# Optimization experiments

Measured on AMD Instinct MI355X. Metric: run time of the kernel, lower is better.

Reference implementation:

```python
import jax, jax.numpy as jnp
import numpy as np

N = 50000      # n_samples (nodes)
F = 128        # n_features
H = 32         # hidden_dim
C = 16         # code_dim
DEG = 32       # avg degree
E = N * DEG + N  # random edges + self loops


def setup_inputs() -> dict:
    key = jax.random.key(0)
    ks = jax.random.split(key, 9)
    src = jax.random.randint(ks[0], (N * DEG,), 0, N, dtype=jnp.int32)
    dst = jax.random.randint(ks[1], (N * DEG,), 0, N, dtype=jnp.int32)
    loops = jnp.arange(N, dtype=jnp.int32)
    edge_src = jnp.concatenate([src, loops])
    edge_dst = jnp.concatenate([dst, loops])
    # symmetric normalization D^{-1/2} (A+I) D^{-1/2} on the edge list
    deg = jax.ops.segment_sum(jnp.ones((E,), jnp.float32), edge_dst, num_segments=N)
    deg = jnp.maximum(deg, 1.0)
    edge_w = jax.lax.rsqrt(deg[edge_src] * deg[edge_dst])
    rand_u = jax.random.uniform(ks[2], (N, C), jnp.float32)  # torch.rand_like
    def w(k, i, o):
        return jax.random.normal(k, (i, o), jnp.float32) * (1.0 / np.sqrt(i))
    return {
        'x': jax.random.normal(ks[3], (N, F), jnp.float32),
        'edge_src': edge_src, 'edge_dst': edge_dst, 'edge_w': edge_w,
        'rand_u': rand_u,
        'W1': w(ks[4], F, H), 'Wm': w(ks[5], H, C), 'Ws': w(ks[6], H, C),
        'Wd': w(ks[7], C, H), 'Wo': w(ks[8], H, F),
    }


def _gcn(x, W, edge_src, edge_dst, edge_w):
    # KipfAndWillingConv: spmm(A_norm, x @ W)
    support = x @ W                               # [N, out]
    msgs = edge_w[:, None] * support[edge_src]    # [E, out]
    return jax.ops.segment_sum(msgs, edge_dst, num_segments=N)


def reference(x, edge_src, edge_dst, edge_w, rand_u, W1, Wm, Ws, Wd, Wo):
    gcn = lambda h, W: _gcn(h, W, edge_src, edge_dst, edge_w)
    hidden = jax.nn.relu(gcn(x, W1))
    means = gcn(hidden, Wm)
    std = jax.nn.elu(gcn(hidden, Ws)) + 1.0
    encoded = means + std * rand_u                # uniform reparameterization
    decoded = jax.nn.relu(gcn(encoded, Wd))
    prediction = jax.nn.relu(gcn(decoded, Wo))
    return (prediction, means, std)
```

## Files before the change

### kernel.cpp

```cpp
#include <hip/hip_runtime.h>
#include <hip/hip_bf16.h>
#include <hip/hip_fp16.h>

typedef unsigned int u32;
typedef unsigned short u16;
typedef unsigned long long u64;

#define NBIN 512
#define BSH 7
#define BCAP 36
#define CHUNK 4096
#define PAD 80
#define NG  (PAD/8)
#define HB 128

__global__ __launch_bounds__(64) void k_init(int* __restrict__ ovf_cnt,
                                             u32* __restrict__ h0, u32* __restrict__ h1,
                                             u32* __restrict__ henc, int N) {
  const int t = threadIdx.x;
  if (t == 0) *ovf_cnt = 0;
  if (t < 16) h0[(size_t)N * 16 + t] = 0;
  if (t < 16) h1[(size_t)N * 16 + t] = 0;
  if (t < 8)  henc[(size_t)N * 8 + t] = 0;
}

__global__ __launch_bounds__(512) void k_bin(const int* __restrict__ src, const int* __restrict__ dst,
                                             int E2, u32* __restrict__ binned, int* __restrict__ blkcnt,
                                             u32* __restrict__ ovf, int* __restrict__ ovf_cnt, int ovfcap) {
  __shared__ int curs[NBIN];
  const int p = blockIdx.x;
  const int base = p * CHUNK;
  const int len = min(CHUNK, E2 - base);
  const int t = threadIdx.x;
  const int lane = t & 63;
  for (int i = t; i < NBIN; i += 512) curs[i] = 0;
  __syncthreads();
  const u32 blkBase = (u32)p * (NBIN * BCAP);
  for (int i = t; i < len; i += 512) {
    int d = dst[base + i];
    u32 e = ((u32)d << 16) | (u32)src[base + i];
    int b = d >> BSH;
    int pos = atomicAdd(&curs[b], 1);
    if (pos < BCAP) binned[blkBase + (u32)b * BCAP + pos] = e;
    u64 om = __ballot(pos >= BCAP);
    if (om) {
      int leader = __ffsll((long long)om) - 1;
      int ob = 0;
      if (lane == leader) ob = atomicAdd(ovf_cnt, (int)__popcll(om));
      ob = __shfl(ob, leader);
      if (pos >= BCAP) {
        int oi = ob + (int)__popcll(om & ((1ull << lane) - 1ull));
        if (oi < ovfcap) ovf[oi] = e;
      }
    }
  }
  __syncthreads();
  for (int b = t; b < NBIN; b += 512) blkcnt[p * NBIN + b] = min(curs[b], BCAP);
}

__global__ __launch_bounds__(512) void k_sort(const u32* __restrict__ binned, const int* __restrict__ blkcnt,
                                              int nblk, const u32* __restrict__ ovf,
                                              const int* __restrict__ ovf_cnt, int N,
                                              u16* __restrict__ csr, int* __restrict__ cur) {
  __shared__ __attribute__((aligned(16))) u16 scsr[HB * PAD];
  __shared__ int cnt[HB];
  const int bin = blockIdx.x;
  const int lo = bin << BSH;
  if (lo >= N) return;
  const int hi = min(lo + HB, N);
  const int H = hi - lo;
  const int t = threadIdx.x;
  const int w = t >> 6, lane = t & 63;
  const u32 sent2 = ((u32)N << 16) | (u32)N;
  for (int i = t; i < HB * PAD / 2; i += 512) ((u32*)scsr)[i] = sent2;
  for (int i = t; i < HB; i += 512) cnt[i] = 0;
  __syncthreads();
  const int per = (nblk + 7) / 8;
  const int c0 = w * per;
  const int c1 = min(nblk, c0 + per);
  const int s = lane >> 3;
  const int k = lane & 7;
  for (int p = c0; p < c1; p += 8) {
    const int myp = p + s;
    int len = 0; u32 sb = 0;
    if (myp < c1) {
      len = blkcnt[myp * NBIN + bin];
      sb = ((u32)myp * NBIN + (u32)bin) * BCAP;
    }
    for (int i = k; i < len; i += 8) {
      u32 e = binned[sb + i];
      int d = (int)(e >> 16);
      int pos = atomicAdd(&cnt[d - lo], 1);
      if (pos < PAD) scsr[(d - lo) * PAD + pos] = (u16)(e & 0xffffu);
    }
  }
  const int onum = min(*ovf_cnt, 1 << 19);
  for (int i = t; i < onum; i += 512) {
    u32 e = ovf[i];
    int d = (int)(e >> 16);
    if (d >= lo && d < hi) {
      int pos = atomicAdd(&cnt[d - lo], 1);
      if (pos < PAD) scsr[(d - lo) * PAD + pos] = (u16)(e & 0xffffu);
    }
  }
  __syncthreads();
  if (H == HB) {
    const uint4* s4 = (const uint4*)scsr;
    uint4* d4 = (uint4*)(csr + (size_t)lo * PAD);
    for (int i = t; i < HB * PAD / 8; i += 512) d4[i] = s4[i];
  } else {
    for (int i = t; i < H * (PAD / 8); i += 512) {
      int node = i / (PAD / 8), q = i % (PAD / 8);
      ((uint4*)(csr + (size_t)(lo + node) * PAD))[q] = ((const uint4*)(scsr + node * PAD))[q];
    }
  }
  for (int i = t; i < H; i += 512) cur[lo + i] = cnt[i];
}

__device__ __forceinline__ void acc8(uint4 v, float* a) {
  const __half2* h = reinterpret_cast<const __half2*>(&v);
#pragma unroll
  for (int p = 0; p < 4; ++p) {
    float2 f = __half22float2(h[p]);
    a[2 * p] += f.x;
    a[2 * p + 1] += f.y;
  }
}
__device__ __forceinline__ uint4 pack8h(const float* v) {
  uint4 r;
  __half2* h = reinterpret_cast<__half2*>(&r);
#pragma unroll
  for (int p = 0; p < 4; ++p) h[p] = __floats2half2_rn(v[2 * p], v[2 * p + 1]);
  return r;
}
__device__ __forceinline__ uint2 pack4h(const float* v) {
  uint2 r;
  __half2* h = reinterpret_cast<__half2*>(&r);
  h[0] = __floats2half2_rn(v[0], v[1]);
  h[1] = __floats2half2_rn(v[2], v[3]);
  return r;
}
__device__ __forceinline__ u32 pack2h(float a, float b) {
  __half2 h = __floats2half2_rn(a, b);
  return *reinterpret_cast<u32*>(&h);
}

template <int LPN, int XD>
__device__ __forceinline__ void gather_split(const u16* __restrict__ csr, const int* __restrict__ cur,
                                             const float* __restrict__ dinv, const uint4* __restrict__ supv,
                                             int g, int cg, int half, float* acc, float& dg_out) {
  const int len = min(cur[g], PAD);
  const u16* c = csr + (size_t)g * PAD;
  ushort4 idx[NG];
#pragma unroll
  for (int j = 0; j < NG; ++j) idx[j] = *(const ushort4*)(c + 8 * j + 4 * half);
#pragma unroll
  for (int p = 0; p < 8; ++p) acc[p] = 0.f;
  if (half == 0) acc8(supv[(size_t)g * LPN + cg], acc);
#pragma unroll
  for (int j = 0; j < NG; ++j) {
    if (8 * j + 4 * half < len) {
      acc8(supv[(size_t)idx[j].x * LPN + cg], acc);
      acc8(supv[(size_t)idx[j].y * LPN + cg], acc);
      acc8(supv[(size_t)idx[j].z * LPN + cg], acc);
      acc8(supv[(size_t)idx[j].w * LPN + cg], acc);
    }
  }
  float dg = dinv[g];
#pragma unroll
  for (int p = 0; p < 8; ++p) acc[p] += __shfl_xor(acc[p], XD);
  dg_out = dg;
#pragma unroll
  for (int p = 0; p < 8; ++p) acc[p] *= dg;
}

__global__ __launch_bounds__(256) void k_spmm_relu(const u16* __restrict__ csr, const int* __restrict__ cur,
                                                   const float* __restrict__ dinv,
                                                   const uint4* __restrict__ sup, uint4* __restrict__ out, int N) {
  int g = blockIdx.x * 32 + (int)(threadIdx.x >> 3);
  int sub = threadIdx.x & 7;
  int half = sub >> 2, cg = sub & 3;
  if (g >= N) return;
  float a[8], dg;
  gather_split<4, 4>(csr, cur, dinv, sup, g, cg, half, a, dg);
  if (half == 0) {
#pragma unroll
    for (int p = 0; p < 8; ++p) a[p] = dg * fmaxf(a[p], 0.f);
    out[(size_t)g * 4 + cg] = pack8h(a);
  }
}

__global__ __launch_bounds__(256) void k_spmm_ms(const u16* __restrict__ csr, const int* __restrict__ cur,
                                                  const float* __restrict__ dinv,
                                                  const uint4* __restrict__ sup,
                                                  const float* __restrict__ Wm, const float* __restrict__ Ws,
                                                  const float* __restrict__ ru,
                                                  u32* __restrict__ enc,
                                                  float* __restrict__ o_means, float* __restrict__ o_std, int N) {
  __shared__ float w[32 * 32];
  __shared__ float aggT[32][33];
  const int t = threadIdx.x;
  for (int i = t; i < 32 * 32; i += 256) {
    int k = i >> 5, j = i & 31;
    w[i] = (j < 16) ? Wm[k * 16 + j] : Ws[k * 16 + (j - 16)];
  }
  const int n = t >> 3;
  const int sub = t & 7;
  const int half = sub >> 2, cg = sub & 3;
  const int g = blockIdx.x * 32 + n;
  const bool act = g < N;
  float dg = 0.f, a[8];
  if (act) {
    gather_split<4, 4>(csr, cur, dinv, sup, g, cg, half, a, dg);
    if (half == 0) {
#pragma unroll
      for (int p = 0; p < 8; ++p) aggT[n][cg * 8 + p] = a[p];
    }
  }
  __syncthreads();
  if (act) {
    const int q = sub;
    float2 rm = make_float2(0.f, 0.f), rs = make_float2(0.f, 0.f);
    for (int k = 0; k < 32; ++k) {
      float rv = aggT[n][k];
      const float2* wr = (const float2*)&w[k * 32];
      float2 wm = wr[q], wsv = wr[8 + q];
      rm.x += rv * wm.x; rm.y += rv * wm.y;
      rs.x += rv * wsv.x; rs.y += rv * wsv.y;
    }
    ((float2*)o_means)[(size_t)g * 8 + q] = rm;
    rs.x = ((rs.x > 0.f) ? rs.x : expm1f(rs.x)) + 1.0f;
    rs.y = ((rs.y > 0.f) ? rs.y : expm1f(rs.y)) + 1.0f;
    ((float2*)o_std)[(size_t)g * 8 + q] = rs;
    float2 uu = ((const float2*)ru)[(size_t)g * 8 + q];
    enc[(size_t)g * 8 + q] = pack2h(dg * (rm.x + rs.x * uu.x), dg * (rm.y + rs.y * uu.y));
  }
}

__global__ __launch_bounds__(256) void k_spmm_d(const u16* __restrict__ csr, const int* __restrict__ cur,
                                                 const float* __restrict__ dinv,
                                                 const uint4* __restrict__ sup,
                                                 const float* __restrict__ Wd,
                                                 uint2* __restrict__ out, int N) {
  __shared__ float w[16 * 32];
  __shared__ float aggT[64][17];
  const int t = threadIdx.x;
  for (int i = t; i < 16 * 32; i += 256) w[i] = Wd[i];
  const int n = t >> 2;
  const int sub = t & 3;
  const int half = sub >> 1, cg = sub & 1;
  const int g = blockIdx.x * 64 + n;
  const bool act = g < N;
  float dg = 0.f, a[8];
  if (act) {
    gather_split<2, 2>(csr, cur, dinv, sup, g, cg, half, a, dg);
    if (half == 0) {
#pragma unroll
      for (int p = 0; p < 8; ++p) aggT[n][cg * 8 + p] = a[p];
    }
  }
  __syncthreads();
  if (act) {
    const int q = sub;
    float4 r0 = make_float4(0.f, 0.f, 0.f, 0.f), r1 = r0;
    for (int k = 0; k < 16; ++k) {
      float rv = aggT[n][k];
      const float4* wr = (const float4*)&w[k * 32];
      float4 w0 = wr[q], w1 = wr[q + 4];
      r0.x += rv * w0.x; r0.y += rv * w0.y; r0.z += rv * w0.z; r0.w += rv * w0.w;
      r1.x += rv * w1.x; r1.y += rv * w1.y; r1.z += rv * w1.z; r1.w += rv * w1.w;
    }
    float v[4];
    v[0] = dg * fmaxf(r0.x, 0.f); v[1] = dg * fmaxf(r0.y, 0.f);
    v[2] = dg * fmaxf(r0.z, 0.f); v[3] = dg * fmaxf(r0.w, 0.f);
    out[(size_t)g * 8 + q] = pack4h(v);
    v[0] = dg * fmaxf(r1.x, 0.f); v[1] = dg * fmaxf(r1.y, 0.f);
    v[2] = dg * fmaxf(r1.z, 0.f); v[3] = dg * fmaxf(r1.w, 0.f);
    out[(size_t)g * 8 + q + 4] = pack4h(v);
  }
}

__global__ __launch_bounds__(256) void k_spmm_o(const u16* __restrict__ csr, const int* __restrict__ cur,
                                                 const float* __restrict__ dinv,
                                                 const uint4* __restrict__ sup,
                                                 const float* __restrict__ Wo,
                                                 float* __restrict__ out, int N) {
  __shared__ float w[32 * 128];
  __shared__ float aggT[32][33];
  const int t = threadIdx.x;
  for (int i = t; i < 32 * 128; i += 256) w[i] = Wo[i];
  const int n = t >> 3;
  const int sub = t & 7;
  const int half = sub >> 2, cg = sub & 3;
  const int g = blockIdx.x * 32 + n;
  const bool act = g < N;
  float dg, a[8];
  if (act) {
    gather_split<4, 4>(csr, cur, dinv, sup, g, cg, half, a, dg);
    if (half == 0) {
#pragma unroll
      for (int p = 0; p < 8; ++p) aggT[n][cg * 8 + p] = a[p];
    }
  }
  __syncthreads();
  if (act) {
    const int q = sub;
    float4 r4[4];
#pragma unroll
    for (int h = 0; h < 4; ++h) r4[h] = make_float4(0.f, 0.f, 0.f, 0.f);
    for (int k = 0; k < 32; ++k) {
      float rv = aggT[n][k];
      const float4* wr = (const float4*)&w[k * 128];
#pragma unroll
      for (int h = 0; h < 4; ++h) {
        float4 wv = wr[q + 8 * h];
        r4[h].x += rv * wv.x; r4[h].y += rv * wv.y;
        r4[h].z += rv * wv.z; r4[h].w += rv * wv.w;
      }
    }
    float4* orow = (float4*)(out + (size_t)g * 128);
#pragma unroll
    for (int h = 0; h < 4; ++h)
      orow[q + 8 * h] = make_float4(fmaxf(r4[h].x, 0.f), fmaxf(r4[h].y, 0.f),
                                    fmaxf(r4[h].z, 0.f), fmaxf(r4[h].w, 0.f));
  }
}

__global__ __launch_bounds__(256) void k_mm1(const float* __restrict__ x, const float* __restrict__ W1,
                                             const int* __restrict__ cur, float* __restrict__ dinv,
                                             uint4* __restrict__ out, int N) {
  __shared__ float w[128 * 32];
  for (int i = threadIdx.x; i < 128 * 32; i += 256) w[i] = W1[i];
  __syncthreads();
  int n = blockIdx.x * 256 + threadIdx.x;
  if (n >= N) return;
  float dn = rsqrtf((float)(cur[n] + 1));
  dinv[n] = dn;
  const float4* xr = (const float4*)(x + (size_t)n * 128);
  float acc[32];
#pragma unroll
  for (int j = 0; j < 32; ++j) acc[j] = 0.f;
  for (int kb = 0; kb < 32; ++kb) {
    float4 p = xr[kb];
    float xe[4] = {p.x, p.y, p.z, p.w};
#pragma unroll
    for (int h = 0; h < 4; ++h) {
      float xv = xe[h];
      const float4* wr = (const float4*)&w[(kb * 4 + h) * 32];
#pragma unroll
      for (int q = 0; q < 8; ++q) {
        float4 a = wr[q];
        acc[q * 4 + 0] += xv * a.x; acc[q * 4 + 1] += xv * a.y;
        acc[q * 4 + 2] += xv * a.z; acc[q * 4 + 3] += xv * a.w;
      }
    }
  }
#pragma unroll
  for (int j = 0; j < 32; ++j) acc[j] *= dn;
  uint4* o = out + (size_t)n * 4;
#pragma unroll
  for (int q = 0; q < 4; ++q) o[q] = pack8h(&acc[q * 8]);
}

extern "C" void kernel_launch(void* const* d_in, const int* in_sizes, int n_in,
                              void* d_out, int out_size, void* d_ws, size_t ws_size,
                              hipStream_t stream) {
  const float* x  = (const float*)d_in[0];
  const int* esrc = (const int*)d_in[1];
  const int* edst = (const int*)d_in[2];
  const float* ru = (const float*)d_in[4];
  const float* W1 = (const float*)d_in[5];
  const float* Wm = (const float*)d_in[6];
  const float* Ws = (const float*)d_in[7];
  const float* Wd = (const float*)d_in[8];
  const float* Wo = (const float*)d_in[9];
  const int N = in_sizes[0] / 128;
  const int E = in_sizes[1];
  const int E2 = E - N;

  const int nblk = (E2 + CHUNK - 1) / CHUNK;
  const int ovfcap = 1 << 19;

  char* ws = (char*)d_ws;
  size_t off = 0;
  auto alloc = [&](size_t bytes) {
    void* p = ws + off;
    off = (off + bytes + 255) & ~(size_t)255;
    return p;
  };
  u16*   csr     = (u16*)alloc((size_t)N * PAD * 2);
  u32*   binned  = (u32*)alloc((size_t)nblk * NBIN * BCAP * 4);
  int*   blkcnt  = (int*)alloc((size_t)nblk * NBIN * 4);
  u32*   ovf     = (u32*)alloc((size_t)ovfcap * 4);
  int*   ovf_cnt = (int*)alloc(256);
  int*   cur     = (int*)alloc((size_t)N * 4);
  float* dinv    = (float*)alloc((size_t)N * 4);
  uint4* h0      = (uint4*)alloc((size_t)(N + 1) * 32 * 2);
  uint4* h1      = (uint4*)alloc((size_t)(N + 1) * 32 * 2);
  u32*   henc    = (u32*)alloc((size_t)(N + 1) * 16 * 2);

  float* out_pred  = (float*)d_out;
  float* out_means = out_pred + (size_t)N * 128;
  float* out_std   = out_means + (size_t)N * 16;

  const int nb = (N + 255) / 256;
  const int sortBlocks = (N + HB - 1) / HB;
  const int g32 = (N + 31) / 32;
  const int g64 = (N + 63) / 64;

  k_init<<<1, 64, 0, stream>>>(ovf_cnt, (u32*)h0, (u32*)h1, henc, N);
  k_bin<<<nblk, 512, 0, stream>>>(esrc, edst, E2, binned, blkcnt, ovf, ovf_cnt, ovfcap);
  k_sort<<<sortBlocks, 512, 0, stream>>>(binned, blkcnt, nblk, ovf, ovf_cnt, N, csr, cur);

  k_mm1<<<nb, 256, 0, stream>>>(x, W1, cur, dinv, h0, N);
  k_spmm_relu<<<g32, 256, 0, stream>>>(csr, cur, dinv, h0, h1, N);
  k_spmm_ms<<<g32, 256, 0, stream>>>(csr, cur, dinv, h1, Wm, Ws, ru,
                                     henc, out_means, out_std, N);
  k_spmm_d<<<g64, 256, 0, stream>>>(csr, cur, dinv, (const uint4*)henc, Wd,
                                    (uint2*)h0, N);
  k_spmm_o<<<g32, 256, 0, stream>>>(csr, cur, dinv, h0, Wo, out_pred, N);
}
```

Baseline: 128.3 us.

## Fuse first matmul into CSR sort kernel and split gathers across four lanes

The x@W1 projection and the degree normalisation are folded into the tail of k_sort. Each block reuses its shared CSR buffer to hold W1 and computes its 128 nodes with four threads per node, combined by lane shuffles. This removes a separate kernel launch and a reread of the degree counts. The SpMM gathers now split each node's neighbour list over four lane groups instead of two, giving more threads and outstanding loads per row, at the cost of an extra shuffle reduction and fewer nodes per block. The epilogue matmuls are redistributed over the extra lanes.

```diff
diff --git a/kernel.cpp b/kernel.cpp
--- a/kernel.cpp
+++ b/kernel.cpp
@@ -11,7 +11,7 @@
 #define BCAP 36
 #define CHUNK 4096
 #define PAD 80
-#define NG  (PAD/8)
+#define NQ 20
 #define HB 128
 
 __global__ __launch_bounds__(64) void k_init(int* __restrict__ ovf_cnt,
@@ -61,7 +61,9 @@
 __global__ __launch_bounds__(512) void k_sort(const u32* __restrict__ binned, const int* __restrict__ blkcnt,
                                               int nblk, const u32* __restrict__ ovf,
                                               const int* __restrict__ ovf_cnt, int N,
-                                              u16* __restrict__ csr, int* __restrict__ cur) {
+                                              u16* __restrict__ csr, int* __restrict__ cur,
+                                              const float* __restrict__ x, const float* __restrict__ W1,
+                                              float* __restrict__ dinv, uint4* __restrict__ s1out) {
   __shared__ __attribute__((aligned(16))) u16 scsr[HB * PAD];
   __shared__ int cnt[HB];
   const int bin = blockIdx.x;
@@ -115,6 +117,50 @@
     }
   }
   for (int i = t; i < H; i += 512) cur[lo + i] = cnt[i];
+  __syncthreads();
+  float* w1 = (float*)scsr;
+  for (int i = t; i < 128 * 32; i += 512) w1[i] = W1[i];
+  __syncthreads();
+  const int n = t >> 2;
+  const int q = t & 2 + (t & 1);
+  if (n < H) {
+    const int g = lo + n;
+    const float4* xr = (const float4*)(x + (size_t)g * 128);
+    float acc[32];
+#pragma unroll
+    for (int j = 0; j < 32; ++j) acc[j] = 0.f;
+#pragma unroll
+    for (int m = 0; m < 8; ++m) {
+      float4 p4 = xr[(t & 3) + 4 * m];
+      float xe[4] = {p4.x, p4.y, p4.z, p4.w};
+#pragma unroll
+      for (int h = 0; h < 4; ++h) {
+        float xv = xe[h];
+        const float4* wr = (const float4*)&w1[(((t & 3) + 4 * m) * 4 + h) * 32];
+#pragma unroll
+        for (int c = 0; c < 8; ++c) {
+          float4 a = wr[c];
+          acc[c * 4 + 0] += xv * a.x; acc[c * 4 + 1] += xv * a.y;
+          acc[c * 4 + 2] += xv * a.z; acc[c * 4 + 3] += xv * a.w;
+        }
+      }
+    }
+#pragma unroll
+    for (int j = 0; j < 32; ++j) {
+      acc[j] += __shfl_xor(acc[j], 1);
+      acc[j] += __shfl_xor(acc[j], 2);
+    }
+    float dn = rsqrtf((float)(cnt[n] + 1));
+    if ((t & 3) == 0) dinv[g] = dn;
+    float v[8];
+#pragma unroll
+    for (int j = 0; j < 8; ++j) v[j] = dn * acc[(t & 3) * 8 + j];
+    uint4 pk;
+    __half2* hh = reinterpret_cast<__half2*>(&pk);
+#pragma unroll
+    for (int p2 = 0; p2 < 4; ++p2) hh[p2] = __floats2half2_rn(v[2 * p2], v[2 * p2 + 1]);
+    s1out[(size_t)g * 4 + (t & 3)] = pk;
+  }
 }
 
 __device__ __forceinline__ void acc8(uint4 v, float* a) {
@@ -145,30 +191,33 @@
   return *reinterpret_cast<u32*>(&h);
 }
 
-template <int LPN, int XD>
-__device__ __forceinline__ void gather_split(const u16* __restrict__ csr, const int* __restrict__ cur,
-                                             const float* __restrict__ dinv, const uint4* __restrict__ supv,
-                                             int g, int cg, int half, float* acc, float& dg_out) {
+template <int LPN>
+__device__ __forceinline__ void gather_quad(const u16* __restrict__ csr, const int* __restrict__ cur,
+                                            const float* __restrict__ dinv, const uint4* __restrict__ supv,
+                                            int g, int cg, int quarter, float* acc, float& dg_out) {
   const int len = min(cur[g], PAD);
   const u16* c = csr + (size_t)g * PAD;
-  ushort4 idx[NG];
-#pragma unroll
-  for (int j = 0; j < NG; ++j) idx[j] = *(const ushort4*)(c + 8 * j + 4 * half);
+  ushort4 idx[5];
+#pragma unroll
+  for (int m = 0; m < 5; ++m) idx[m] = *(const ushort4*)(c + 4 * (quarter + 4 * m));
 #pragma unroll
   for (int p = 0; p < 8; ++p) acc[p] = 0.f;
-  if (half == 0) acc8(supv[(size_t)g * LPN + cg], acc);
-#pragma unroll
-  for (int j = 0; j < NG; ++j) {
-    if (8 * j + 4 * half < len) {
-      acc8(supv[(size_t)idx[j].x * LPN + cg], acc);
-      acc8(supv[(size_t)idx[j].y * LPN + cg], acc);
-      acc8(supv[(size_t)idx[j].z * LPN + cg], acc);
-      acc8(supv[(size_t)idx[j].w * LPN + cg], acc);
+  if (quarter == 0) acc8(supv[(size_t)g * LPN + cg], acc);
+#pragma unroll
+  for (int m = 0; m < 5; ++m) {
+    if (4 * (quarter + 4 * m) < len) {
+      acc8(supv[(size_t)idx[m].x * LPN + cg], acc);
+      acc8(supv[(size_t)idx[m].y * LPN + cg], acc);
+      acc8(supv[(size_t)idx[m].z * LPN + cg], acc);
+      acc8(supv[(size_t)idx[m].w * LPN + cg], acc);
     }
   }
   float dg = dinv[g];
 #pragma unroll
-  for (int p = 0; p < 8; ++p) acc[p] += __shfl_xor(acc[p], XD);
+  for (int p = 0; p < 8; ++p) {
+    acc[p] += __shfl_xor(acc[p], LPN);
+    acc[p] += __shfl_xor(acc[p], 2 * LPN);
+  }
   dg_out = dg;
 #pragma unroll
   for (int p = 0; p < 8; ++p) acc[p] *= dg;
@@ -177,13 +226,13 @@
 __global__ __launch_bounds__(256) void k_spmm_relu(const u16* __restrict__ csr, const int* __restrict__ cur,
                                                    const float* __restrict__ dinv,
                                                    const uint4* __restrict__ sup, uint4* __restrict__ out, int N) {
-  int g = blockIdx.x * 32 + (int)(threadIdx.x >> 3);
-  int sub = threadIdx.x & 7;
-  int half = sub >> 2, cg = sub & 3;
+  int g = blockIdx.x * 16 + (int)(threadIdx.x >> 4);
+  int sub = threadIdx.x & 15;
+  int quarter = sub >> 2, cg = sub & 3;
   if (g >= N) return;
   float a[8], dg;
-  gather_split<4, 4>(csr, cur, dinv, sup, g, cg, half, a, dg);
-  if (half == 0) {
+  gather_quad<4>(csr, cur, dinv, sup, g, cg, quarter, a, dg);
+  if (quarter == 0) {
 #pragma unroll
     for (int p = 0; p < 8; ++p) a[p] = dg * fmaxf(a[p], 0.f);
     out[(size_t)g * 4 + cg] = pack8h(a);
@@ -198,27 +247,27 @@
                                                   u32* __restrict__ enc,
                                                   float* __restrict__ o_means, float* __restrict__ o_std, int N) {
   __shared__ float w[32 * 32];
-  __shared__ float aggT[32][33];
+  __shared__ float aggT[16][33];
   const int t = threadIdx.x;
   for (int i = t; i < 32 * 32; i += 256) {
     int k = i >> 5, j = i & 31;
     w[i] = (j < 16) ? Wm[k * 16 + j] : Ws[k * 16 + (j - 16)];
   }
-  const int n = t >> 3;
-  const int sub = t & 7;
-  const int half = sub >> 2, cg = sub & 3;
-  const int g = blockIdx.x * 32 + n;
+  const int n = t >> 4;
+  const int sub = t & 15;
+  const int quarter = sub >> 2, cg = sub & 3;
+  const int g = blockIdx.x * 16 + n;
   const bool act = g < N;
   float dg = 0.f, a[8];
   if (act) {
-    gather_split<4, 4>(csr, cur, dinv, sup, g, cg, half, a, dg);
-    if (half == 0) {
+    gather_quad<4>(csr, cur, dinv, sup, g, cg, quarter, a, dg);
+    if (quarter == 0) {
 #pragma unroll
       for (int p = 0; p < 8; ++p) aggT[n][cg * 8 + p] = a[p];
     }
   }
   __syncthreads();
-  if (act) {
+  if (act && sub < 8) {
     const int q = sub;
     float2 rm = make_float2(0.f, 0.f), rs = make_float2(0.f, 0.f);
     for (int k = 0; k < 32; ++k) {
@@ -243,18 +292,18 @@
                                                  const float* __restrict__ Wd,
                                                  uint2* __restrict__ out, int N) {
   __shared__ float w[16 * 32];
-  __shared__ float aggT[64][17];
+  __shared__ float aggT[32][17];
   const int t = threadIdx.x;
   for (int i = t; i < 16 * 32; i += 256) w[i] = Wd[i];
-  const int n = t >> 2;
-  const int sub = t & 3;
-  const int half = sub >> 1, cg = sub & 1;
-  const int g = blockIdx.x * 64 + n;
+  const int n = t >> 3;
+  const int sub = t & 7;
+  const int quarter = sub >> 1, cg = sub & 1;
+  const int g = blockIdx.x * 32 + n;
   const bool act = g < N;
   float dg = 0.f, a[8];
   if (act) {
-    gather_split<2, 2>(csr, cur, dinv, sup, g, cg, half, a, dg);
-    if (half == 0) {
+    gather_quad<2>(csr, cur, dinv, sup, g, cg, quarter, a, dg);
+    if (quarter == 0) {
 #pragma unroll
       for (int p = 0; p < 8; ++p) aggT[n][cg * 8 + p] = a[p];
     }
@@ -262,21 +311,16 @@
   __syncthreads();
   if (act) {
     const int q = sub;
-    float4 r0 = make_float4(0.f, 0.f, 0.f, 0.f), r1 = r0;
+    float4 r0 = make_float4(0.f, 0.f, 0.f, 0.f);
     for (int k = 0; k < 16; ++k) {
       float rv = aggT[n][k];
-      const float4* wr = (const float4*)&w[k * 32];
-      float4 w0 = wr[q], w1 = wr[q + 4];
+      float4 w0 = ((const float4*)&w[k * 32])[q];
       r0.x += rv * w0.x; r0.y += rv * w0.y; r0.z += rv * w0.z; r0.w += rv * w0.w;
-      r1.x += rv * w1.x; r1.y += rv * w1.y; r1.z += rv * w1.z; r1.w += rv * w1.w;
     }
     float v[4];
     v[0] = dg * fmaxf(r0.x, 0.f); v[1] = dg * fmaxf(r0.y, 0.f);
     v[2] = dg * fmaxf(r0.z, 0.f); v[3] = dg * fmaxf(r0.w, 0.f);
     out[(size_t)g * 8 + q] = pack4h(v);
-    v[0] = dg * fmaxf(r1.x, 0.f); v[1] = dg * fmaxf(r1.y, 0.f);
-    v[2] = dg * fmaxf(r1.z, 0.f); v[3] = dg * fmaxf(r1.w, 0.f);
-    out[(size_t)g * 8 + q + 4] = pack4h(v);
   }
 }
 
@@ -286,18 +330,18 @@
                                                  const float* __restrict__ Wo,
                                                  float* __restrict__ out, int N) {
   __shared__ float w[32 * 128];
-  __shared__ float aggT[32][33];
+  __shared__ float aggT[16][33];
   const int t = threadIdx.x;
   for (int i = t; i < 32 * 128; i += 256) w[i] = Wo[i];
-  const int n = t >> 3;
-  const int sub = t & 7;
-  const int half = sub >> 2, cg = sub & 3;
-  const int g = blockIdx.x * 32 + n;
+  const int n = t >> 4;
+  const int sub = t & 15;
+  const int quarter = sub >> 2, cg = sub & 3;
+  const int g = blockIdx.x * 16 + n;
   const bool act = g < N;
   float dg, a[8];
   if (act) {
-    gather_split<4, 4>(csr, cur, dinv, sup, g, cg, half, a, dg);
-    if (half == 0) {
+    gather_quad<4>(csr, cur, dinv, sup, g, cg, quarter, a, dg);
+    if (quarter == 0) {
 #pragma unroll
       for (int p = 0; p < 8; ++p) aggT[n][cg * 8 + p] = a[p];
     }
@@ -305,61 +349,22 @@
   __syncthreads();
   if (act) {
     const int q = sub;
-    float4 r4[4];
-#pragma unroll
-    for (int h = 0; h < 4; ++h) r4[h] = make_float4(0.f, 0.f, 0.f, 0.f);
+    float4 r4[2];
+    r4[0] = make_float4(0.f, 0.f, 0.f, 0.f);
+    r4[1] = r4[0];
     for (int k = 0; k < 32; ++k) {
       float rv = aggT[n][k];
       const float4* wr = (const float4*)&w[k * 128];
-#pragma unroll
-      for (int h = 0; h < 4; ++h) {
-        float4 wv = wr[q + 8 * h];
-        r4[h].x += rv * wv.x; r4[h].y += rv * wv.y;
-        r4[h].z += rv * wv.z; r4[h].w += rv * wv.w;
-      }
+      float4 w0 = wr[q], w1 = wr[q + 16];
+      r4[0].x += rv * w0.x; r4[0].y += rv * w0.y; r4[0].z += rv * w0.z; r4[0].w += rv * w0.w;
+      r4[1].x += rv * w1.x; r4[1].y += rv * w1.y; r4[1].z += rv * w1.z; r4[1].w += rv * w1.w;
     }
     float4* orow = (float4*)(out + (size_t)g * 128);
-#pragma unroll
-    for (int h = 0; h < 4; ++h)
-      orow[q + 8 * h] = make_float4(fmaxf(r4[h].x, 0.f), fmaxf(r4[h].y, 0.f),
-                                    fmaxf(r4[h].z, 0.f), fmaxf(r4[h].w, 0.f));
-  }
-}
-
-__global__ __launch_bounds__(256) void k_mm1(const float* __restrict__ x, const float* __restrict__ W1,
-                                             const int* __restrict__ cur, float* __restrict__ dinv,
-                                             uint4* __restrict__ out, int N) {
-  __shared__ float w[128 * 32];
-  for (int i = threadIdx.x; i < 128 * 32; i += 256) w[i] = W1[i];
-  __syncthreads();
-  int n = blockIdx.x * 256 + threadIdx.x;
-  if (n >= N) return;
-  float dn = rsqrtf((float)(cur[n] + 1));
-  dinv[n] = dn;
-  const float4* xr = (const float4*)(x + (size_t)n * 128);
-  float acc[32];
-#pragma unroll
-  for (int j = 0; j < 32; ++j) acc[j] = 0.f;
-  for (int kb = 0; kb < 32; ++kb) {
-    float4 p = xr[kb];
-    float xe[4] = {p.x, p.y, p.z, p.w};
-#pragma unroll
-    for (int h = 0; h < 4; ++h) {
-      float xv = xe[h];
-      const float4* wr = (const float4*)&w[(kb * 4 + h) * 32];
-#pragma unroll
-      for (int q = 0; q < 8; ++q) {
-        float4 a = wr[q];
-        acc[q * 4 + 0] += xv * a.x; acc[q * 4 + 1] += xv * a.y;
-        acc[q * 4 + 2] += xv * a.z; acc[q * 4 + 3] += xv * a.w;
-      }
-    }
-  }
-#pragma unroll
-  for (int j = 0; j < 32; ++j) acc[j] *= dn;
-  uint4* o = out + (size_t)n * 4;
-#pragma unroll
-  for (int q = 0; q < 4; ++q) o[q] = pack8h(&acc[q * 8]);
+    orow[q]      = make_float4(fmaxf(r4[0].x, 0.f), fmaxf(r4[0].y, 0.f),
+                               fmaxf(r4[0].z, 0.f), fmaxf(r4[0].w, 0.f));
+    orow[q + 16] = make_float4(fmaxf(r4[1].x, 0.f), fmaxf(r4[1].y, 0.f),
+                               fmaxf(r4[1].z, 0.f), fmaxf(r4[1].w, 0.f));
+  }
 }
 
 extern "C" void kernel_launch(void* const* d_in, const int* in_sizes, int n_in,
@@ -403,20 +408,18 @@
   float* out_means = out_pred + (size_t)N * 128;
   float* out_std   = out_means + (size_t)N * 16;
 
-  const int nb = (N + 255) / 256;
   const int sortBlocks = (N + HB - 1) / HB;
+  const int g16 = (N + 15) / 16;
   const int g32 = (N + 31) / 32;
-  const int g64 = (N + 63) / 64;
 
   k_init<<<1, 64, 0, stream>>>(ovf_cnt, (u32*)h0, (u32*)h1, henc, N);
   k_bin<<<nblk, 512, 0, stream>>>(esrc, edst, E2, binned, blkcnt, ovf, ovf_cnt, ovfcap);
-  k_sort<<<sortBlocks, 512, 0, stream>>>(binned, blkcnt, nblk, ovf, ovf_cnt, N, csr, cur);
-
-  k_mm1<<<nb, 256, 0, stream>>>(x, W1, cur, dinv, h0, N);
-  k_spmm_relu<<<g32, 256, 0, stream>>>(csr, cur, dinv, h0, h1, N);
-  k_spmm_ms<<<g32, 256, 0, stream>>>(csr, cur, dinv, h1, Wm, Ws, ru,
+  k_sort<<<sortBlocks, 512, 0, stream>>>(binned, blkcnt, nblk, ovf, ovf_cnt, N, csr, cur,
+                                         x, W1, dinv, h0);
+  k_spmm_relu<<<g16, 256, 0, stream>>>(csr, cur, dinv, h0, h1, N);
+  k_spmm_ms<<<g16, 256, 0, stream>>>(csr, cur, dinv, h1, Wm, Ws, ru,
                                      henc, out_means, out_std, N);
-  k_spmm_d<<<g64, 256, 0, stream>>>(csr, cur, dinv, (const uint4*)henc, Wd,
+  k_spmm_d<<<g32, 256, 0, stream>>>(csr, cur, dinv, (const uint4*)henc, Wd,
                                     (uint2*)h0, N);
-  k_spmm_o<<<g32, 256, 0, stream>>>(csr, cur, dinv, h0, Wo, out_pred, N);
-}
+  k_spmm_o<<<g16, 256, 0, stream>>>(csr, cur, dinv, h0, Wo, out_pred, N);
+}
```

After: 141.8 us. +10.5%, slower.

## Replicate feature buffers eight ways per XCD and use nontemporal loads/stores

Applied to the files above, without the earlier changes.

Each producer kernel writes up to eight copies of its fp16 feature matrix. Each consumer block reads the copy chosen by blockIdx&7, which under round-robin dispatch maps blocks to XCDs so each die's L2 holds its own replica. CSR index loads and output stores become nontemporal so streaming data does not evict the gathered features from cache. The init kernel is replaced by a memset plus zeroing of pad rows inside the producers. This costs extra write traffic and workspace, and the replica-to-XCD mapping rests on an assumed dispatch order.

```diff
diff --git a/kernel.cpp b/kernel.cpp
--- a/kernel.cpp
+++ b/kernel.cpp
@@ -5,6 +5,11 @@
 typedef unsigned int u32;
 typedef unsigned short u16;
 typedef unsigned long long u64;
+typedef u16   us4n __attribute__((ext_vector_type(4)));
+typedef u32   ui4n __attribute__((ext_vector_type(4)));
+typedef u32   ui2n __attribute__((ext_vector_type(2)));
+typedef float f2n  __attribute__((ext_vector_type(2)));
+typedef float f4n  __attribute__((ext_vector_type(4)));
 
 #define NBIN 512
 #define BSH 7
@@ -13,16 +18,6 @@
 #define PAD 80
 #define NG  (PAD/8)
 #define HB 128
-
-__global__ __launch_bounds__(64) void k_init(int* __restrict__ ovf_cnt,
-                                             u32* __restrict__ h0, u32* __restrict__ h1,
-                                             u32* __restrict__ henc, int N) {
-  const int t = threadIdx.x;
-  if (t == 0) *ovf_cnt = 0;
-  if (t < 16) h0[(size_t)N * 16 + t] = 0;
-  if (t < 16) h1[(size_t)N * 16 + t] = 0;
-  if (t < 8)  henc[(size_t)N * 8 + t] = 0;
-}
 
 __global__ __launch_bounds__(512) void k_bin(const int* __restrict__ src, const int* __restrict__ dst,
                                              int E2, u32* __restrict__ binned, int* __restrict__ blkcnt,
@@ -133,16 +128,15 @@
   for (int p = 0; p < 4; ++p) h[p] = __floats2half2_rn(v[2 * p], v[2 * p + 1]);
   return r;
 }
-__device__ __forceinline__ uint2 pack4h(const float* v) {
-  uint2 r;
-  __half2* h = reinterpret_cast<__half2*>(&r);
-  h[0] = __floats2half2_rn(v[0], v[1]);
-  h[1] = __floats2half2_rn(v[2], v[3]);
-  return r;
-}
 __device__ __forceinline__ u32 pack2h(float a, float b) {
   __half2 h = __floats2half2_rn(a, b);
   return *reinterpret_cast<u32*>(&h);
+}
+__device__ __forceinline__ void nst4(uint4 v, uint4* p) {
+  __builtin_nontemporal_store(*reinterpret_cast<ui4n*>(&v), reinterpret_cast<ui4n*>(p));
+}
+__device__ __forceinline__ void nst2(uint2 v, uint2* p) {
+  __builtin_nontemporal_store(*reinterpret_cast<ui2n*>(&v), reinterpret_cast<ui2n*>(p));
 }
 
 template <int LPN, int XD>
@@ -151,9 +145,10 @@
                                              int g, int cg, int half, float* acc, float& dg_out) {
   const int len = min(cur[g], PAD);
   const u16* c = csr + (size_t)g * PAD;
-  ushort4 idx[NG];
-#pragma unroll
-  for (int j = 0; j < NG; ++j) idx[j] = *(const ushort4*)(c + 8 * j + 4 * half);
+  us4n idx[NG];
+#pragma unroll
+  for (int j = 0; j < NG; ++j)
+    idx[j] = __builtin_nontemporal_load((const us4n*)(c + 8 * j + 4 * half));
 #pragma unroll
   for (int p = 0; p < 8; ++p) acc[p] = 0.f;
   if (half == 0) acc8(supv[(size_t)g * LPN + cg], acc);
@@ -176,17 +171,22 @@
 
 __global__ __launch_bounds__(256) void k_spmm_relu(const u16* __restrict__ csr, const int* __restrict__ cur,
                                                    const float* __restrict__ dinv,
-                                                   const uint4* __restrict__ sup, uint4* __restrict__ out, int N) {
+                                                   const uint4* __restrict__ sup, uint4* __restrict__ out,
+                                                   int N, int rep, size_t s4) {
+  const int copy = (int)(blockIdx.x & 7) & (rep - 1);
+  if (blockIdx.x == 0 && threadIdx.x < 16)
+    for (int r = 0; r < rep; ++r) ((u32*)out)[r * s4 * 4 + (size_t)N * 16 + threadIdx.x] = 0;
   int g = blockIdx.x * 32 + (int)(threadIdx.x >> 3);
   int sub = threadIdx.x & 7;
   int half = sub >> 2, cg = sub & 3;
   if (g >= N) return;
   float a[8], dg;
-  gather_split<4, 4>(csr, cur, dinv, sup, g, cg, half, a, dg);
+  gather_split<4, 4>(csr, cur, dinv, sup + (size_t)copy * s4, g, cg, half, a, dg);
   if (half == 0) {
 #pragma unroll
     for (int p = 0; p < 8; ++p) a[p] = dg * fmaxf(a[p], 0.f);
-    out[(size_t)g * 4 + cg] = pack8h(a);
+    uint4 v = pack8h(a);
+    for (int r = 0; r < rep; ++r) nst4(v, out + r * s4 + (size_t)g * 4 + cg);
   }
 }
 
@@ -196,10 +196,14 @@
                                                   const float* __restrict__ Wm, const float* __restrict__ Ws,
                                                   const float* __restrict__ ru,
                                                   u32* __restrict__ enc,
-                                                  float* __restrict__ o_means, float* __restrict__ o_std, int N) {
+                                                  float* __restrict__ o_means, float* __restrict__ o_std,
+                                                  int N, int rep, size_t s4, size_t e32) {
   __shared__ float w[32 * 32];
   __shared__ float aggT[32][33];
   const int t = threadIdx.x;
+  const int copy = (int)(blockIdx.x & 7) & (rep - 1);
+  if (blockIdx.x == 0 && t < 8)
+    for (int r = 0; r < rep; ++r) enc[r * e32 + (size_t)N * 8 + t] = 0;
   for (int i = t; i < 32 * 32; i += 256) {
     int k = i >> 5, j = i & 31;
     w[i] = (j < 16) ? Wm[k * 16 + j] : Ws[k * 16 + (j - 16)];
@@ -211,7 +215,7 @@
   const bool act = g < N;
   float dg = 0.f, a[8];
   if (act) {
-    gather_split<4, 4>(csr, cur, dinv, sup, g, cg, half, a, dg);
+    gather_split<4, 4>(csr, cur, dinv, sup + (size_t)copy * s4, g, cg, half, a, dg);
     if (half == 0) {
 #pragma unroll
       for (int p = 0; p < 8; ++p) aggT[n][cg * 8 + p] = a[p];
@@ -228,12 +232,16 @@
       rm.x += rv * wm.x; rm.y += rv * wm.y;
       rs.x += rv * wsv.x; rs.y += rv * wsv.y;
     }
-    ((float2*)o_means)[(size_t)g * 8 + q] = rm;
+    f2n vm = {rm.x, rm.y};
+    __builtin_nontemporal_store(vm, (f2n*)((float2*)o_means + (size_t)g * 8 + q));
     rs.x = ((rs.x > 0.f) ? rs.x : expm1f(rs.x)) + 1.0f;
     rs.y = ((rs.y > 0.f) ? rs.y : expm1f(rs.y)) + 1.0f;
-    ((float2*)o_std)[(size_t)g * 8 + q] = rs;
+    f2n vs = {rs.x, rs.y};
+    __builtin_nontemporal_store(vs, (f2n*)((float2*)o_std + (size_t)g * 8 + q));
     float2 uu = ((const float2*)ru)[(size_t)g * 8 + q];
-    enc[(size_t)g * 8 + q] = pack2h(dg * (rm.x + rs.x * uu.x), dg * (rm.y + rs.y * uu.y));
+    u32 ev = pack2h(dg * (rm.x + rs.x * uu.x), dg * (rm.y + rs.y * uu.y));
+    for (int r = 0; r < rep; ++r)
+      __builtin_nontemporal_store(ev, &enc[r * e32 + (size_t)g * 8 + q]);
   }
 }
 
@@ -241,10 +249,12 @@
                                                  const float* __restrict__ dinv,
                                                  const uint4* __restrict__ sup,
                                                  const float* __restrict__ Wd,
-                                                 uint2* __restrict__ out, int N) {
+                                                 uint2* __restrict__ out,
+                                                 int N, int rep, size_t e4, size_t d2) {
   __shared__ float w[16 * 32];
   __shared__ float aggT[64][17];
   const int t = threadIdx.x;
+  const int copy = (int)(blockIdx.x & 7) & (rep - 1);
   for (int i = t; i < 16 * 32; i += 256) w[i] = Wd[i];
   const int n = t >> 2;
   const int sub = t & 3;
@@ -253,7 +263,7 @@
   const bool act = g < N;
   float dg = 0.f, a[8];
   if (act) {
-    gather_split<2, 2>(csr, cur, dinv, sup, g, cg, half, a, dg);
+    gather_split<2, 2>(csr, cur, dinv, sup + (size_t)copy * e4, g, cg, half, a, dg);
     if (half == 0) {
 #pragma unroll
       for (int p = 0; p < 8; ++p) aggT[n][cg * 8 + p] = a[p];
@@ -270,13 +280,23 @@
       r0.x += rv * w0.x; r0.y += rv * w0.y; r0.z += rv * w0.z; r0.w += rv * w0.w;
       r1.x += rv * w1.x; r1.y += rv * w1.y; r1.z += rv * w1.z; r1.w += rv * w1.w;
     }
-    float v[4];
-    v[0] = dg * fmaxf(r0.x, 0.f); v[1] = dg * fmaxf(r0.y, 0.f);
-    v[2] = dg * fmaxf(r0.z, 0.f); v[3] = dg * fmaxf(r0.w, 0.f);
-    out[(size_t)g * 8 + q] = pack4h(v);
-    v[0] = dg * fmaxf(r1.x, 0.f); v[1] = dg * fmaxf(r1.y, 0.f);
-    v[2] = dg * fmaxf(r1.z, 0.f); v[3] = dg * fmaxf(r1.w, 0.f);
-    out[(size_t)g * 8 + q + 4] = pack4h(v);
+    uint2 o0, o1;
+    {
+      float v[4] = {dg * fmaxf(r0.x, 0.f), dg * fmaxf(r0.y, 0.f),
+                    dg * fmaxf(r0.z, 0.f), dg * fmaxf(r0.w, 0.f)};
+      __half2* h = reinterpret_cast<__half2*>(&o0);
+      h[0] = __floats2half2_rn(v[0], v[1]); h[1] = __floats2half2_rn(v[2], v[3]);
+    }
+    {
+      float v[4] = {dg * fmaxf(r1.x, 0.f), dg * fmaxf(r1.y, 0.f),
+                    dg * fmaxf(r1.z, 0.f), dg * fmaxf(r1.w, 0.f)};
+      __half2* h = reinterpret_cast<__half2*>(&o1);
+      h[0] = __floats2half2_rn(v[0], v[1]); h[1] = __floats2half2_rn(v[2], v[3]);
+    }
+    for (int r = 0; r < rep; ++r) {
+      nst2(o0, out + r * d2 + (size_t)g * 8 + q);
+      nst2(o1, out + r * d2 + (size_t)g * 8 + q + 4);
+    }
   }
 }
 
@@ -284,10 +304,12 @@
                                                  const float* __restrict__ dinv,
                                                  const uint4* __restrict__ sup,
                                                  const float* __restrict__ Wo,
-                                                 float* __restrict__ out, int N) {
+                                                 float* __restrict__ out,
+                                                 int N, int rep, size_t s4) {
   __shared__ float w[32 * 128];
   __shared__ float aggT[32][33];
   const int t = threadIdx.x;
+  const int copy = (int)(blockIdx.x & 7) & (rep - 1);
   for (int i = t; i < 32 * 128; i += 256) w[i] = Wo[i];
   const int n = t >> 3;
   const int sub = t & 7;
@@ -296,7 +318,7 @@
   const bool act = g < N;
   float dg, a[8];
   if (act) {
-    gather_split<4, 4>(csr, cur, dinv, sup, g, cg, half, a, dg);
+    gather_split<4, 4>(csr, cur, dinv, sup + (size_t)copy * s4, g, cg, half, a, dg);
     if (half == 0) {
 #pragma unroll
       for (int p = 0; p < 8; ++p) aggT[n][cg * 8 + p] = a[p];
@@ -320,16 +342,20 @@
     }
     float4* orow = (float4*)(out + (size_t)g * 128);
 #pragma unroll
-    for (int h = 0; h < 4; ++h)
-      orow[q + 8 * h] = make_float4(fmaxf(r4[h].x, 0.f), fmaxf(r4[h].y, 0.f),
-                                    fmaxf(r4[h].z, 0.f), fmaxf(r4[h].w, 0.f));
+    for (int h = 0; h < 4; ++h) {
+      f4n v = {fmaxf(r4[h].x, 0.f), fmaxf(r4[h].y, 0.f),
+               fmaxf(r4[h].z, 0.f), fmaxf(r4[h].w, 0.f)};
+      __builtin_nontemporal_store(v, (f4n*)&orow[q + 8 * h]);
+    }
   }
 }
 
 __global__ __launch_bounds__(256) void k_mm1(const float* __restrict__ x, const float* __restrict__ W1,
                                              const int* __restrict__ cur, float* __restrict__ dinv,
-                                             uint4* __restrict__ out, int N) {
+                                             uint4* __restrict__ out, int N, int rep, size_t s4) {
   __shared__ float w[128 * 32];
+  if (blockIdx.x == 0 && threadIdx.x < 16)
+    for (int r = 0; r < rep; ++r) ((u32*)out)[r * s4 * 4 + (size_t)N * 16 + threadIdx.x] = 0;
   for (int i = threadIdx.x; i < 128 * 32; i += 256) w[i] = W1[i];
   __syncthreads();
   int n = blockIdx.x * 256 + threadIdx.x;
@@ -357,9 +383,11 @@
   }
 #pragma unroll
   for (int j = 0; j < 32; ++j) acc[j] *= dn;
-  uint4* o = out + (size_t)n * 4;
-#pragma unroll
-  for (int q = 0; q < 4; ++q) o[q] = pack8h(&acc[q * 8]);
+#pragma unroll
+  for (int q = 0; q < 4; ++q) {
+    uint4 v = pack8h(&acc[q * 8]);
+    for (int r = 0; r < rep; ++r) nst4(v, out + r * s4 + (size_t)n * 4 + q);
+  }
 }
 
 extern "C" void kernel_launch(void* const* d_in, const int* in_sizes, int n_in,
@@ -380,6 +408,7 @@
 
   const int nblk = (E2 + CHUNK - 1) / CHUNK;
   const int ovfcap = 1 << 19;
+  const size_t rows = (size_t)N + 1;
 
   char* ws = (char*)d_ws;
   size_t off = 0;
@@ -395,9 +424,16 @@
   int*   ovf_cnt = (int*)alloc(256);
   int*   cur     = (int*)alloc((size_t)N * 4);
   float* dinv    = (float*)alloc((size_t)N * 4);
-  uint4* h0      = (uint4*)alloc((size_t)(N + 1) * 32 * 2);
-  uint4* h1      = (uint4*)alloc((size_t)(N + 1) * 32 * 2);
-  u32*   henc    = (u32*)alloc((size_t)(N + 1) * 16 * 2);
+
+  const size_t featOne = rows * 64 * 2 + rows * 32;
+  const int rep = (ws_size >= off + 8 * featOne + (1u << 20)) ? 8 : 1;
+  uint4* h0   = (uint4*)alloc((size_t)rep * rows * 64);
+  uint4* h1   = (uint4*)alloc((size_t)rep * rows * 64);
+  u32*   henc = (u32*)alloc((size_t)rep * rows * 32);
+  const size_t s4  = rows * 4;
+  const size_t e32 = rows * 8;
+  const size_t e4  = rows * 2;
+  const size_t d2  = rows * 8;
 
   float* out_pred  = (float*)d_out;
   float* out_means = out_pred + (size_t)N * 128;
@@ -408,15 +444,15 @@
   const int g32 = (N + 31) / 32;
   const int g64 = (N + 63) / 64;
 
-  k_init<<<1, 64, 0, stream>>>(ovf_cnt, (u32*)h0, (u32*)h1, henc, N);
+  hipMemsetAsync(ovf_cnt, 0, 4, stream);
   k_bin<<<nblk, 512, 0, stream>>>(esrc, edst, E2, binned, blkcnt, ovf, ovf_cnt, ovfcap);
   k_sort<<<sortBlocks, 512, 0, stream>>>(binned, blkcnt, nblk, ovf, ovf_cnt, N, csr, cur);
 
-  k_mm1<<<nb, 256, 0, stream>>>(x, W1, cur, dinv, h0, N);
-  k_spmm_relu<<<g32, 256, 0, stream>>>(csr, cur, dinv, h0, h1, N);
+  k_mm1<<<nb, 256, 0, stream>>>(x, W1, cur, dinv, h0, N, rep, s4);
+  k_spmm_relu<<<g32, 256, 0, stream>>>(csr, cur, dinv, h0, h1, N, rep, s4);
   k_spmm_ms<<<g32, 256, 0, stream>>>(csr, cur, dinv, h1, Wm, Ws, ru,
-                                     henc, out_means, out_std, N);
+                                     henc, out_means, out_std, N, rep, s4, e32);
   k_spmm_d<<<g64, 256, 0, stream>>>(csr, cur, dinv, (const uint4*)henc, Wd,
-                                    (uint2*)h0, N);
-  k_spmm_o<<<g32, 256, 0, stream>>>(csr, cur, dinv, h0, Wo, out_pred, N);
-}
+                                    (uint2*)h0, N, rep, e4, d2);
+  k_spmm_o<<<g32, 256, 0, stream>>>(csr, cur, dinv, h0, Wo, out_pred, N, rep, s4);
+}
```

Result: slower. 188.0 us (+46.6%).
